# Performance work log

Measured on AMD Instinct MI355X. Metric: run time of the kernel, lower is better.

Reference implementation:

```python
import jax, jax.numpy as jnp
import numpy as np

IN_F, OUT_F, N_CLASSES, HEADS = 512, 64, 40, 4
B, M = 1, 4096
NEG_SLOPE = 0.01  # F.leaky_relu called with default slope (self.alpha unused)


def _xavier(key, shape, gain=1.0):
    fan_in, fan_out = shape[-1], shape[-2] if len(shape) > 1 else shape[-1]
    a = gain * np.sqrt(6.0 / (fan_in + fan_out))
    return jax.random.uniform(key, shape, jnp.float32, -a, a)


def setup_inputs() -> dict:
    key = jax.random.key(0)
    ks = jax.random.split(key, 12)
    h = jax.random.normal(ks[0], (B, M, IN_F), jnp.float32)
    A = jax.random.randint(ks[1], (B, M, M), 0, 2, jnp.int32)
    A = jnp.maximum(A, jnp.eye(M, dtype=jnp.int32)[None])  # self-loops avoid empty softmax rows
    return {
        "h": h,
        "A": A,
        "W1_w": _xavier(ks[2], (OUT_F * HEADS, IN_F)),
        "W1_b": jnp.zeros((OUT_F * HEADS,), jnp.float32),
        "a1": _xavier(ks[3], (HEADS, 2 * OUT_F), gain=1.414),
        "W3_w": _xavier(ks[4], (OUT_F, OUT_F * HEADS)),
        "W3_b": jnp.zeros((OUT_F,), jnp.float32),
        "W2_w": _xavier(ks[5], (OUT_F * HEADS, OUT_F)),
        "W2_b": jnp.zeros((OUT_F * HEADS,), jnp.float32),
        "a2": _xavier(ks[6], (HEADS, 2 * OUT_F)),
        "FL_w": _xavier(ks[7], (N_CLASSES, OUT_F * HEADS)),
        "FL_b": jnp.zeros((N_CLASSES,), jnp.float32),
    }


def _attention_block(h, mask, W_w, W_b, a):
    # h: (b,m,n); mask: (b,m,m) bool; W_w: (heads*out, n); a: (heads, 2*out)
    b, m, _ = h.shape
    Wh = jnp.einsum('bmn,on->bmo', h, W_w) + W_b          # (b,m,heads*out)
    Wh = Wh.reshape(b, m, HEADS, -1)                       # (b,m,h,c)
    c = Wh.shape[-1]
    src = jnp.einsum('bmhc,hc->bmh', Wh, a[:, :c])         # score from edge source i
    dst = jnp.einsum('bmhc,hc->bmh', Wh, a[:, c:])         # score from edge target j
    logits = jax.nn.leaky_relu(src[:, :, None, :] + dst[:, None, :, :], NEG_SLOPE)  # (b,i,j,h)
    logits = jnp.where(mask[..., None], logits, -jnp.inf)
    probs = jax.nn.softmax(logits, axis=2)                 # softmax over neighbors j
    out = jnp.einsum('bijh,bjhc->bihc', probs, Wh)
    return out.reshape(b, m, HEADS * c)


def reference(h, A, W1_w, W1_b, a1, W3_w, W3_b, W2_w, W2_b, a2, FL_w, FL_b):
    mask = A == 1
    x = _attention_block(h, mask, W1_w, W1_b, a1)          # (b,m,heads*out)
    x = jnp.einsum('bmo,po->bmp', x, W3_w) + W3_b          # (b,m,out)
    x = _attention_block(x, mask, W2_w, W2_b, a2)          # (b,m,heads*out)
    out = jnp.einsum('bmo,ko->bmk', x, FL_w) + FL_b        # (b,m,n_classes)
    return (x, out)
```

## Files before the change

kernel.cpp:

```cpp
#include <hip/hip_runtime.h>
#include <hip/hip_bf16.h>

typedef _Float16 f16_t;
typedef unsigned short u16;
typedef unsigned int u32;
typedef float f32x4 __attribute__((ext_vector_type(4)));
typedef f16_t f16x8 __attribute__((ext_vector_type(8)));
typedef u16 u16x8 __attribute__((ext_vector_type(8)));
typedef u16 u16x4 __attribute__((ext_vector_type(4)));

#define MROWS 4096
#define NHEADS 4
#define COUT 64
#define OHF 256
#define NCLS 40
#define LOG2E 1.4426950408889634f
#define PLD 264

static __device__ __forceinline__ u16 f16b(float x) {
    return __builtin_bit_cast(u16, (f16_t)x);
}
static __device__ __forceinline__ float f16f(u16 x) {
    return (float)__builtin_bit_cast(f16_t, x);
}
static __device__ __forceinline__ float dmu_decode(u32 ku) {
    const u32 fb = (ku & 0x80000000u) ? (ku ^ 0x80000000u) : ~ku;
    return __builtin_bit_cast(float, fb);
}

__global__ __launch_bounds__(256) void init_kernel(const int* __restrict__ A,
                                                   u32* __restrict__ AbitsT,
                                                   const float* __restrict__ W1w,
                                                   const float* __restrict__ W1b,
                                                   const float* __restrict__ a1,
                                                   const float* __restrict__ W2w,
                                                   const float* __restrict__ W2b,
                                                   const float* __restrict__ W3w,
                                                   const float* __restrict__ W3b,
                                                   const float* __restrict__ a2,
                                                   float* __restrict__ Cwf,
                                                   float* __restrict__ cbf,
                                                   float* __restrict__ va1,
                                                   float* __restrict__ vc1,
                                                   float* __restrict__ va2,
                                                   float* __restrict__ vc2,
                                                   u32* __restrict__ dmu) {
    __shared__ u32 W[2][128];
    __shared__ float u[8][64];
    const int bx = blockIdx.x, tid = threadIdx.x;
    if (bx < 2048) {
        const int i0 = bx * 2;
        const int lane = tid & 63, wv = tid >> 6;
        for (int t = wv; t < 32; t += 4) {
            const int r = t >> 4, q = t & 15;
            const size_t base = (size_t)(i0 + r) * MROWS + q * 256 + lane;
            const int a0 = A[base];
            const int a1_ = A[base + 64];
            const int a2_ = A[base + 128];
            const int a3 = A[base + 192];
            const unsigned long long b0 = __ballot(a0 != 0);
            const unsigned long long b1 = __ballot(a1_ != 0);
            const unsigned long long b2 = __ballot(a2_ != 0);
            const unsigned long long b3 = __ballot(a3 != 0);
            if (lane == 0) {
                W[r][q * 8 + 0] = (u32)b0;
                W[r][q * 8 + 2] = (u32)b1;
                W[r][q * 8 + 4] = (u32)b2;
                W[r][q * 8 + 6] = (u32)b3;
            } else if (lane == 1) {
                W[r][q * 8 + 1] = (u32)(b0 >> 32);
                W[r][q * 8 + 3] = (u32)(b1 >> 32);
                W[r][q * 8 + 5] = (u32)(b2 >> 32);
                W[r][q * 8 + 7] = (u32)(b3 >> 32);
            }
        }
        __syncthreads();
        {
            const int jw = tid >> 1, r = tid & 1;
            AbitsT[(size_t)jw * MROWS + i0 + r] = W[r][jw];
        }
        return;
    }
    const int bid = bx - 2048;
    if (bid < 256) {
        float acc = 0.f;
        for (int t = 0; t < 64; ++t)
            acc += W2w[bid * 64 + t] * W3w[t * 256 + tid];
        Cwf[bid * 256 + tid] = acc;
        if (tid == 0) {
            float b = 0.f;
            for (int t = 0; t < 64; ++t) b += W2w[bid * 64 + t] * W3b[t];
            cbf[bid] = b + W2b[bid];
        }
    } else if (bid < 258) {
        const int k = (bid - 256) * 256 + tid;
#pragma unroll
        for (int hs = 0; hs < 8; ++hs) {
            const int h = hs >> 1, s = hs & 1;
            float acc = 0.f;
            for (int c = 0; c < COUT; ++c)
                acc += W1w[(size_t)(h * COUT + c) * 512 + k] * a1[h * 128 + s * COUT + c];
            va1[hs * 512 + k] = acc;
        }
        if (bid == 256 && tid == 0) {
            for (int hs = 0; hs < 8; ++hs) {
                const int h = hs >> 1, s = hs & 1;
                float b = 0.f;
                for (int c = 0; c < COUT; ++c) b += W1b[h * COUT + c] * a1[h * 128 + s * COUT + c];
                vc1[hs] = b;
            }
        }
    } else if (bid == 258) {
#pragma unroll
        for (int e = tid * 2; e < tid * 2 + 2; ++e) {
            const int hs = e >> 6, t = e & 63;
            const int h = hs >> 1, s = hs & 1;
            float acc = 0.f;
            for (int c = 0; c < COUT; ++c)
                acc += W2w[(size_t)(h * COUT + c) * 64 + t] * a2[h * 128 + s * COUT + c];
            u[hs][t] = acc;
        }
        __syncthreads();
#pragma unroll
        for (int hs = 0; hs < 8; ++hs) {
            float acc = 0.f;
            for (int t = 0; t < 64; ++t) acc += u[hs][t] * W3w[t * 256 + tid];
            va2[hs * 256 + tid] = acc;
        }
        if (tid == 0) {
            for (int hs = 0; hs < 8; ++hs) {
                const int h = hs >> 1, s = hs & 1;
                float b = 0.f;
                for (int t = 0; t < 64; ++t) b += u[hs][t] * W3b[t];
                for (int c = 0; c < COUT; ++c) b += W2b[h * COUT + c] * a2[h * 128 + s * COUT + c];
                vc2[hs] = b;
            }
        }
    } else {
        if (tid < 8) dmu[tid] = 0u;
    }
}

__global__ __launch_bounds__(256) void proj_kernel(const float* __restrict__ X,
                                                   const float* __restrict__ Bm,
                                                   const float* __restrict__ bias,
                                                   int K,
                                                   u16* __restrict__ WhT,
                                                   const float* __restrict__ va,
                                                   const float* __restrict__ vc,
                                                   float* __restrict__ srcT,
                                                   float* __restrict__ dstT,
                                                   u32* __restrict__ dmu) {
    __shared__ u16 Al[64][40];
    __shared__ u16 Bl[64][40];
    __shared__ float red[16][16][9];
    __shared__ float dred[4][16];
    const int tid = threadIdx.x;
    if (blockIdx.x < 256) {
        const int lane = tid & 63, wv = tid >> 6;
        const int l15 = lane & 15, g = lane >> 4;
        const int m0 = (blockIdx.x & 63) * 64, n0 = (blockIdx.x >> 6) * 64;
        const int r = tid >> 2, c8 = (tid & 3) * 8;
        f32x4 acc[4] = {};
        for (int k0 = 0; k0 < K; k0 += 32) {
            const float4 a0 = *(const float4*)&X[(size_t)(m0 + r) * K + k0 + c8];
            const float4 a1 = *(const float4*)&X[(size_t)(m0 + r) * K + k0 + c8 + 4];
            const float4 b0 = *(const float4*)&Bm[(size_t)(n0 + r) * K + k0 + c8];
            const float4 b1 = *(const float4*)&Bm[(size_t)(n0 + r) * K + k0 + c8 + 4];
            u16x8 av, bv;
            av[0] = f16b(a0.x); av[1] = f16b(a0.y); av[2] = f16b(a0.z); av[3] = f16b(a0.w);
            av[4] = f16b(a1.x); av[5] = f16b(a1.y); av[6] = f16b(a1.z); av[7] = f16b(a1.w);
            bv[0] = f16b(b0.x); bv[1] = f16b(b0.y); bv[2] = f16b(b0.z); bv[3] = f16b(b0.w);
            bv[4] = f16b(b1.x); bv[5] = f16b(b1.y); bv[6] = f16b(b1.z); bv[7] = f16b(b1.w);
            __syncthreads();
            *(u16x8*)&Al[r][c8] = av;
            *(u16x8*)&Bl[r][c8] = bv;
            __syncthreads();
            f16x8 afr = *(const f16x8*)&Al[16 * wv + l15][8 * g];
#pragma unroll
            for (int ni = 0; ni < 4; ++ni) {
                f16x8 bfr = *(const f16x8*)&Bl[16 * ni + l15][8 * g];
                acc[ni] = __builtin_amdgcn_mfma_f32_16x16x32_f16(afr, bfr, acc[ni], 0, 0, 0);
            }
        }
#pragma unroll
        for (int ni = 0; ni < 4; ++ni) {
            const int n = n0 + 16 * ni + l15;
            const float bvs = bias[n];
            u16x4 pv;
#pragma unroll
            for (int rr = 0; rr < 4; ++rr) pv[rr] = f16b(acc[ni][rr] + bvs);
            *(u16x4*)&WhT[(size_t)n * MROWS + m0 + 16 * wv + 4 * g] = pv;
        }
        return;
    }
    const int bs = blockIdx.x - 256;
    const int ii = tid >> 4, ki = tid & 15;
    const int i = bs * 16 + ii;
    const int KS = K >> 4;
    const int k0 = ki * KS;
    float acc[8] = {};
    for (int k = k0; k < k0 + KS; k += 4) {
        const float4 xv = *(const float4*)&X[(size_t)i * K + k];
#pragma unroll
        for (int hs = 0; hs < 8; ++hs) {
            const float4 vv = *(const float4*)&va[(size_t)hs * K + k];
            acc[hs] += xv.x * vv.x + xv.y * vv.y + xv.z * vv.z + xv.w * vv.w;
        }
    }
#pragma unroll
    for (int hs = 0; hs < 8; ++hs) red[ii][ki][hs] = acc[hs];
    __syncthreads();
    if (tid < 128) {
        const int row = tid >> 3, hs = tid & 7, h = hs >> 1;
        float sum = 0.f;
#pragma unroll
        for (int kk = 0; kk < 16; ++kk) sum += red[row][kk][hs];
        const float val = sum + vc[hs];
        const int ig = bs * 16 + row;
        if ((hs & 1) == 0) {
            srcT[h * MROWS + ig] = val;
        } else {
            dstT[h * MROWS + ig] = val;
            dred[h][row] = val;
        }
    }
    __syncthreads();
    if (tid < 4) {
        float m = -3.4e38f;
#pragma unroll
        for (int r = 0; r < 16; ++r) m = fmaxf(m, dred[tid][r]);
        const u32 b = __builtin_bit_cast(u32, m);
        const u32 key = (b & 0x80000000u) ? ~b : (b | 0x80000000u);
        atomicMax(dmu + tid, key);
    }
}

template <int JT>
__global__ __launch_bounds__(512) void attn_kernel(const u16* __restrict__ WhT,
                                                   const float* __restrict__ srcT,
                                                   const float* __restrict__ dstT,
                                                   const u32* __restrict__ AbitsT,
                                                   const u32* __restrict__ dmu,
                                                   u16* __restrict__ partial,
                                                   float* __restrict__ outF) {
    constexpr int J64 = JT * 64;
    __shared__ __align__(16) unsigned char whL[256 * 128];
    __shared__ __align__(16) float GT[8 * J64];
    const int tid = threadIdx.x;
    const int lane = tid & 63, w = tid >> 6;
    const int h = w & 3, half = w >> 2;
    const int l15 = lane & 15, g = lane >> 4;
    const int i0 = blockIdx.x * 64;
    const int chunk = blockIdx.y;
    const int jbase = chunk * J64;
    const int xorm = (l15 & 7) << 4;

    for (int e = tid; e < 8 * J64; e += 512) {
        const int hb = e / J64;
        const int j = e - hb * J64;
        const float dmhe = dmu_decode(dmu[hb >> 1]);
        const float sc = (hb & 1) ? 0.01f * LOG2E : LOG2E;
        GT[e] = __builtin_amdgcn_exp2f((dstT[(hb >> 1) * MROWS + jbase + j] - dmhe) * sc);
    }

    const float dmh = dmu_decode(dmu[h]);
    float negs_[2], F1_[2], F2_[2];
#pragma unroll
    for (int mi = 0; mi < 2; ++mi) {
        const float s = srcT[h * MROWS + i0 + 32 * half + 16 * mi + l15];
        const float sd = s + dmh;
        const float C = fmaxf(sd, 0.01f * sd);
        negs_[mi] = -s;
        F1_[mi] = __builtin_amdgcn_exp2f((sd - C) * LOG2E);
        F2_[mi] = __builtin_amdgcn_exp2f((0.01f * sd - C) * LOG2E);
    }

    f32x4 acc[2][4] = {};
    f32x4 acc1[2] = {};
    f16x8 ones;
#pragma unroll
    for (int e = 0; e < 8; ++e) ones[e] = (f16_t)1.0f;

    for (int jt = 0; jt < JT; ++jt) {
        const int j0 = jbase + jt * 64;
        __syncthreads();
#pragma unroll
        for (int q = 0; q < 4; ++q) {
            const int eid = tid + 512 * q;
            const int c = eid >> 3, jo8 = eid & 7;
            u16x8 v = *(const u16x8*)&WhT[(size_t)c * MROWS + j0 + jo8 * 8];
            *(u16x8*)(whL + c * 128 + ((jo8 * 16) ^ ((c & 7) << 4))) = v;
        }
        __syncthreads();
        f16x8 af[2];
#pragma unroll
        for (int kj = 0; kj < 2; ++kj) {
            const int jk = j0 + 32 * kj + 8 * g;
            const float4 d0 = *(const float4*)&dstT[h * MROWS + jk];
            const float4 d1 = *(const float4*)&dstT[h * MROWS + jk + 4];
            float dv[8] = {d0.x, d0.y, d0.z, d0.w, d1.x, d1.y, d1.z, d1.w};
            const int goff = jt * 64 + 32 * kj + 8 * g;
            const float4 g10 = *(const float4*)&GT[(h * 2) * J64 + goff];
            const float4 g11 = *(const float4*)&GT[(h * 2) * J64 + goff + 4];
            const float4 g20 = *(const float4*)&GT[(h * 2 + 1) * J64 + goff];
            const float4 g21 = *(const float4*)&GT[(h * 2 + 1) * J64 + goff + 4];
            const float G1[8] = {g10.x, g10.y, g10.z, g10.w, g11.x, g11.y, g11.z, g11.w};
            const float G2[8] = {g20.x, g20.y, g20.z, g20.w, g21.x, g21.y, g21.z, g21.w};
#pragma unroll
            for (int mi = 0; mi < 2; ++mi) {
                const int irow = i0 + 32 * half + 16 * mi + l15;
                const u32 word = AbitsT[(size_t)((j0 >> 5) + kj) * MROWS + irow];
                const u32 bits = (word >> (8 * g)) & 0xffu;
                f16x8 a;
#pragma unroll
                for (int e = 0; e < 8; ++e) {
                    const bool pos = dv[e] >= negs_[mi];
                    float wv = (pos ? G1[e] : G2[e]) * (pos ? F1_[mi] : F2_[mi]);
                    wv = ((bits >> e) & 1u) ? wv : 0.f;
                    a[e] = (f16_t)wv;
                }
                af[mi] = a;
            }
#pragma unroll
            for (int ni = 0; ni < 4; ++ni) {
                const int c = h * COUT + 16 * ni + l15;
                f16x8 b = *(const f16x8*)(whL + c * 128 + ((64 * kj + 16 * g) ^ xorm));
                acc[0][ni] = __builtin_amdgcn_mfma_f32_16x16x32_f16(af[0], b, acc[0][ni], 0, 0, 0);
                acc[1][ni] = __builtin_amdgcn_mfma_f32_16x16x32_f16(af[1], b, acc[1][ni], 0, 0, 0);
            }
            acc1[0] = __builtin_amdgcn_mfma_f32_16x16x32_f16(af[0], ones, acc1[0], 0, 0, 0);
            acc1[1] = __builtin_amdgcn_mfma_f32_16x16x32_f16(af[1], ones, acc1[1], 0, 0, 0);
        }
    }

    if (partial) {
        u16* pc = partial + (size_t)chunk * MROWS * PLD;
#pragma unroll
        for (int mi = 0; mi < 2; ++mi) {
#pragma unroll
            for (int ni = 0; ni < 4; ++ni)
#pragma unroll
                for (int rr = 0; rr < 4; ++rr) {
                    const int i = i0 + 32 * half + 16 * mi + 4 * g + rr;
                    pc[(size_t)i * PLD + h * COUT + 16 * ni + l15] = f16b(acc[mi][ni][rr]);
                }
#pragma unroll
            for (int rr = 0; rr < 4; ++rr)
                if (l15 == rr)
                    pc[(size_t)(i0 + 32 * half + 16 * mi + 4 * g + rr) * PLD + 256 + h] =
                        f16b(acc1[mi][rr]);
        }
    } else {
#pragma unroll
        for (int mi = 0; mi < 2; ++mi)
#pragma unroll
            for (int rr = 0; rr < 4; ++rr) {
                const int i = i0 + 32 * half + 16 * mi + 4 * g + rr;
                const float rs = acc1[mi][rr];
#pragma unroll
                for (int ni = 0; ni < 4; ++ni)
                    outF[(size_t)i * OHF + h * COUT + 16 * ni + l15] = acc[mi][ni][rr] / rs;
            }
    }
}

__global__ __launch_bounds__(256) void combine_kernel(const u16* __restrict__ partial,
                                                      int nchunk,
                                                      float* __restrict__ outF,
                                                      const float* __restrict__ FLw,
                                                      const float* __restrict__ FLb,
                                                      float* __restrict__ outL) {
    __shared__ float xrow[256];
    __shared__ float cred[40][4];
    const int i = blockIdx.x, c = threadIdx.x, h = c >> 6;
    float v = 0.f, rs = 0.f;
    for (int ch = 0; ch < nchunk; ++ch) {
        const u16* pc = partial + (size_t)ch * MROWS * PLD + (size_t)i * PLD;
        v += f16f(pc[c]);
        rs += f16f(pc[256 + h]);
    }
    const float r = v / rs;
    outF[(size_t)i * OHF + c] = r;
    if (!FLw) return;
    xrow[c] = r;
    __syncthreads();
    if (c < 160) {
        const int k = c >> 2, seg = c & 3;
        const float* xp = &xrow[seg * 64];
        const float* wp = &FLw[(size_t)k * OHF + seg * 64];
        float a = 0.f;
#pragma unroll
        for (int t = 0; t < 64; t += 4) {
            const float4 x4 = *(const float4*)&xp[t];
            const float4 w4 = *(const float4*)&wp[t];
            a += x4.x * w4.x + x4.y * w4.y + x4.z * w4.z + x4.w * w4.w;
        }
        cred[k][seg] = a;
    }
    __syncthreads();
    if (c < NCLS)
        outL[(size_t)i * NCLS + c] = cred[c][0] + cred[c][1] + cred[c][2] + cred[c][3] + FLb[c];
}

extern "C" void kernel_launch(void* const* d_in, const int* in_sizes, int n_in,
                              void* d_out, int out_size, void* d_ws, size_t ws_size,
                              hipStream_t stream) {
    const float* hIn = (const float*)d_in[0];
    const int*   A   = (const int*)d_in[1];
    const float* W1w = (const float*)d_in[2];
    const float* W1b = (const float*)d_in[3];
    const float* a1  = (const float*)d_in[4];
    const float* W3w = (const float*)d_in[5];
    const float* W3b = (const float*)d_in[6];
    const float* W2w = (const float*)d_in[7];
    const float* W2b = (const float*)d_in[8];
    const float* a2  = (const float*)d_in[9];
    const float* FLw = (const float*)d_in[10];
    const float* FLb = (const float*)d_in[11];
    float* outX = (float*)d_out;
    float* outL = outX + (size_t)MROWS * OHF;

    char* p = (char*)d_ws;
    auto alloc = [&](size_t bytes) { char* q = p; p += (bytes + 255) & ~(size_t)255; return q; };
    u32*   AbitsT = (u32*)alloc((size_t)MROWS * 128 * 4);
    u16*   WhT1  = (u16*)alloc((size_t)OHF * MROWS * 2);
    u16*   WhT2  = (u16*)alloc((size_t)OHF * MROWS * 2);
    float* x1f   = (float*)alloc((size_t)MROWS * OHF * 4);
    float* Cwf   = (float*)alloc((size_t)256 * 256 * 4);
    float* cbf   = (float*)alloc(256 * 4);
    float* va1   = (float*)alloc((size_t)8 * 512 * 4);
    float* vc1   = (float*)alloc(8 * 4);
    float* va2   = (float*)alloc((size_t)8 * 256 * 4);
    float* vc2   = (float*)alloc(8 * 4);
    float* srcT1 = (float*)alloc((size_t)NHEADS * MROWS * 4);
    float* dstT1 = (float*)alloc((size_t)NHEADS * MROWS * 4);
    float* srcT2 = (float*)alloc((size_t)NHEADS * MROWS * 4);
    float* dstT2 = (float*)alloc((size_t)NHEADS * MROWS * 4);
    u32*   dmu   = (u32*)alloc(8 * 4);
    size_t fixed = (size_t)(p - (char*)d_ws);
    int nchunk = 8;
    if (fixed + (size_t)8 * MROWS * PLD * 2 > ws_size) nchunk = 4;
    u16* partial = (u16*)p;

    dim3 blk(256);
    init_kernel<<<dim3(2308), blk, 0, stream>>>(A, AbitsT, W1w, W1b, a1, W2w, W2b,
                                                W3w, W3b, a2, Cwf, cbf, va1, vc1,
                                                va2, vc2, dmu);

    auto launch_attn = [&](const u16* WhT, const float* srcT, const float* dstT,
                           const u32* dm) {
        if (nchunk == 8)
            attn_kernel<8><<<dim3(64, 8), dim3(512), 0, stream>>>(WhT, srcT, dstT, AbitsT, dm, partial, nullptr);
        else
            attn_kernel<16><<<dim3(64, 4), dim3(512), 0, stream>>>(WhT, srcT, dstT, AbitsT, dm, partial, nullptr);
    };

    proj_kernel<<<dim3(512), blk, 0, stream>>>(hIn, W1w, W1b, 512, WhT1,
                                               va1, vc1, srcT1, dstT1, dmu);
    launch_attn(WhT1, srcT1, dstT1, dmu);
    combine_kernel<<<dim3(4096), blk, 0, stream>>>(partial, nchunk, x1f,
                                                   nullptr, nullptr, nullptr);

    proj_kernel<<<dim3(512), blk, 0, stream>>>(x1f, Cwf, cbf, 256, WhT2,
                                               va2, vc2, srcT2, dstT2, dmu + 4);
    launch_attn(WhT2, srcT2, dstT2, dmu + 4);
    combine_kernel<<<dim3(4096), blk, 0, stream>>>(partial, nchunk, outX,
                                                   FLw, FLb, outL);
}
```

Measured before the change: 183.5 us.

## Store projected Wh in MFMA-fragment layout and read B operands directly from global

Result: no change. 181.8 us (-0.9%).

```diff
diff --git a/kernel.cpp b/kernel.cpp
--- a/kernel.cpp
+++ b/kernel.cpp
@@ -145,7 +145,7 @@
                                                    const float* __restrict__ Bm,
                                                    const float* __restrict__ bias,
                                                    int K,
-                                                   u16* __restrict__ WhT,
+                                                   u16* __restrict__ WhF,
                                                    const float* __restrict__ va,
                                                    const float* __restrict__ vc,
                                                    float* __restrict__ srcT,
@@ -153,6 +153,7 @@
                                                    u32* __restrict__ dmu) {
     __shared__ u16 Al[64][40];
     __shared__ u16 Bl[64][40];
+    __shared__ u16 Tl[64][72];
     __shared__ float red[16][16][9];
     __shared__ float dred[4][16];
     const int tid = threadIdx.x;
@@ -185,12 +186,21 @@
         }
 #pragma unroll
         for (int ni = 0; ni < 4; ++ni) {
-            const int n = n0 + 16 * ni + l15;
-            const float bvs = bias[n];
-            u16x4 pv;
-#pragma unroll
-            for (int rr = 0; rr < 4; ++rr) pv[rr] = f16b(acc[ni][rr] + bvs);
-            *(u16x4*)&WhT[(size_t)n * MROWS + m0 + 16 * wv + 4 * g] = pv;
+            const int nl = 16 * ni + l15;
+            const float bvs = bias[n0 + nl];
+#pragma unroll
+            for (int rr = 0; rr < 4; ++rr)
+                Tl[nl][16 * wv + 4 * g + rr] = f16b(acc[ni][rr] + bvs);
+        }
+        __syncthreads();
+        const int jb0 = m0 >> 5;
+#pragma unroll
+        for (int q = 0; q < 2; ++q) {
+            const int id = tid + 256 * q;
+            const int jb_l = id >> 8, rem = id & 255;
+            const int c_l = rem >> 2, gf = rem & 3;
+            u16x8 v = *(const u16x8*)&Tl[c_l][32 * jb_l + 8 * gf];
+            *(u16x8*)&WhF[(size_t)(((jb0 + jb_l) * 256 + n0 + c_l) * 4 + gf) * 8] = v;
         }
         return;
     }
@@ -237,7 +247,7 @@
 }
 
 template <int JT>
-__global__ __launch_bounds__(512) void attn_kernel(const u16* __restrict__ WhT,
+__global__ __launch_bounds__(512) void attn_kernel(const u16* __restrict__ WhF,
                                                    const float* __restrict__ srcT,
                                                    const float* __restrict__ dstT,
                                                    const u32* __restrict__ AbitsT,
@@ -245,7 +255,6 @@
                                                    u16* __restrict__ partial,
                                                    float* __restrict__ outF) {
     constexpr int J64 = JT * 64;
-    __shared__ __align__(16) unsigned char whL[256 * 128];
     __shared__ __align__(16) float GT[8 * J64];
     const int tid = threadIdx.x;
     const int lane = tid & 63, w = tid >> 6;
@@ -254,7 +263,6 @@
     const int i0 = blockIdx.x * 64;
     const int chunk = blockIdx.y;
     const int jbase = chunk * J64;
-    const int xorm = (l15 & 7) << 4;
 
     for (int e = tid; e < 8 * J64; e += 512) {
         const int hb = e / J64;
@@ -275,6 +283,7 @@
         F1_[mi] = __builtin_amdgcn_exp2f((sd - C) * LOG2E);
         F2_[mi] = __builtin_amdgcn_exp2f((0.01f * sd - C) * LOG2E);
     }
+    __syncthreads();
 
     f32x4 acc[2][4] = {};
     f32x4 acc1[2] = {};
@@ -284,15 +293,6 @@
 
     for (int jt = 0; jt < JT; ++jt) {
         const int j0 = jbase + jt * 64;
-        __syncthreads();
-#pragma unroll
-        for (int q = 0; q < 4; ++q) {
-            const int eid = tid + 512 * q;
-            const int c = eid >> 3, jo8 = eid & 7;
-            u16x8 v = *(const u16x8*)&WhT[(size_t)c * MROWS + j0 + jo8 * 8];
-            *(u16x8*)(whL + c * 128 + ((jo8 * 16) ^ ((c & 7) << 4))) = v;
-        }
-        __syncthreads();
         f16x8 af[2];
 #pragma unroll
         for (int kj = 0; kj < 2; ++kj) {
@@ -322,10 +322,11 @@
                 }
                 af[mi] = a;
             }
+            const int jb = (j0 >> 5) + kj;
 #pragma unroll
             for (int ni = 0; ni < 4; ++ni) {
                 const int c = h * COUT + 16 * ni + l15;
-                f16x8 b = *(const f16x8*)(whL + c * 128 + ((64 * kj + 16 * g) ^ xorm));
+                f16x8 b = *(const f16x8*)&WhF[(size_t)(((jb << 8) + c) * 4 + g) * 8];
                 acc[0][ni] = __builtin_amdgcn_mfma_f32_16x16x32_f16(af[0], b, acc[0][ni], 0, 0, 0);
                 acc[1][ni] = __builtin_amdgcn_mfma_f32_16x16x32_f16(af[1], b, acc[1][ni], 0, 0, 0);
             }
@@ -424,8 +425,8 @@
     char* p = (char*)d_ws;
     auto alloc = [&](size_t bytes) { char* q = p; p += (bytes + 255) & ~(size_t)255; return q; };
     u32*   AbitsT = (u32*)alloc((size_t)MROWS * 128 * 4);
-    u16*   WhT1  = (u16*)alloc((size_t)OHF * MROWS * 2);
-    u16*   WhT2  = (u16*)alloc((size_t)OHF * MROWS * 2);
+    u16*   WhF1  = (u16*)alloc((size_t)OHF * MROWS * 2);
+    u16*   WhF2  = (u16*)alloc((size_t)OHF * MROWS * 2);
     float* x1f   = (float*)alloc((size_t)MROWS * OHF * 4);
     float* Cwf   = (float*)alloc((size_t)256 * 256 * 4);
     float* cbf   = (float*)alloc(256 * 4);
@@ -448,23 +449,23 @@
                                                 W3w, W3b, a2, Cwf, cbf, va1, vc1,
                                                 va2, vc2, dmu);
 
-    auto launch_attn = [&](const u16* WhT, const float* srcT, const float* dstT,
+    auto launch_attn = [&](const u16* WhF, const float* srcT, const float* dstT,
                            const u32* dm) {
         if (nchunk == 8)
-            attn_kernel<8><<<dim3(64, 8), dim3(512), 0, stream>>>(WhT, srcT, dstT, AbitsT, dm, partial, nullptr);
+            attn_kernel<8><<<dim3(64, 8), dim3(512), 0, stream>>>(WhF, srcT, dstT, AbitsT, dm, partial, nullptr);
         else
-            attn_kernel<16><<<dim3(64, 4), dim3(512), 0, stream>>>(WhT, srcT, dstT, AbitsT, dm, partial, nullptr);
+            attn_kernel<16><<<dim3(64, 4), dim3(512), 0, stream>>>(WhF, srcT, dstT, AbitsT, dm, partial, nullptr);
     };
 
-    proj_kernel<<<dim3(512), blk, 0, stream>>>(hIn, W1w, W1b, 512, WhT1,
+    proj_kernel<<<dim3(512), blk, 0, stream>>>(hIn, W1w, W1b, 512, WhF1,
                                                va1, vc1, srcT1, dstT1, dmu);
-    launch_attn(WhT1, srcT1, dstT1, dmu);
+    launch_attn(WhF1, srcT1, dstT1, dmu);
     combine_kernel<<<dim3(4096), blk, 0, stream>>>(partial, nchunk, x1f,
                                                    nullptr, nullptr, nullptr);
 
-    proj_kernel<<<dim3(512), blk, 0, stream>>>(x1f, Cwf, cbf, 256, WhT2,
+    proj_kernel<<<dim3(512), blk, 0, stream>>>(x1f, Cwf, cbf, 256, WhF2,
                                                va2, vc2, srcT2, dstT2, dmu + 4);
-    launch_attn(WhT2, srcT2, dstT2, dmu + 4);
+    launch_attn(WhF2, srcT2, dstT2, dmu + 4);
     combine_kernel<<<dim3(4096), blk, 0, stream>>>(partial, nchunk, outX,
                                                    FLw, FLb, outL);
 }
```
